# Kernel tuning notes

Hardware: AMD Instinct MI355X
Metric: run time of the kernel (lower is better)

## Reference

```python
import jax, jax.numpy as jnp
import numpy as np

B, S, H, I, E, K = 1, 2048, 1024, 2048, 8, 2


def setup_inputs() -> dict:
    key = jax.random.key(0)
    k0, k1, k2, k3, k4 = jax.random.split(key, 5)
    x = jax.random.normal(k0, (B, S, H), dtype=jnp.float32)
    Wg = jax.random.normal(k1, (H, E), dtype=jnp.float32) * 0.02   # gate (no bias)
    W1 = jax.random.normal(k2, (E, H, I), dtype=jnp.float32) * 0.02  # expert up
    W3 = jax.random.normal(k3, (E, H, I), dtype=jnp.float32) * 0.02  # expert gate
    W2 = jax.random.normal(k4, (E, I, H), dtype=jnp.float32) * 0.02  # expert down
    return {"x": x, "Wg": Wg, "W1": W1, "W2": W2, "W3": W3}


def reference(x, Wg, W1, W2, W3):
    b, s, h = x.shape
    e = Wg.shape[1]
    xf = x.reshape(-1, h)                      # (T, H)
    T = xf.shape[0]

    # Router: top-2 logits, softmax over the 2 selected logits (fp32), cast back.
    logits = xf @ Wg                           # (T, E)
    top_vals, top_idx = jax.lax.top_k(logits, K)
    rw = jax.nn.softmax(top_vals.astype(jnp.float32), axis=-1).astype(x.dtype)  # (T, K)

    # Dense per-expert combine weight: w[t, e] = routing weight if expert e selected, else 0.
    w = jnp.zeros((T, e), dtype=x.dtype).at[jnp.arange(T)[:, None], top_idx].add(rw)

    # Expert MLPs computed for all experts, zero-weighted tokens contribute nothing
    # (mathematically identical to the gather/MLP/scatter-add in the torch loop).
    up = jnp.einsum('th,ehi->tei', xf, W1)     # (T, E, I)
    gate = jnp.einsum('th,ehi->tei', xf, W3)   # (T, E, I)
    act = jax.nn.silu(up) * gate               # (T, E, I)
    out = jnp.einsum('tei,eih,te->th', act, W2, w)  # (T, H)
    return out.reshape(b, s, h)
```

## Files before the change

kernel.cpp:

```cpp
#include <hip/hip_runtime.h>
#include <math.h>

#define NUM_TOK 2048
#define HDIM 1024
#define IDIM 2048
#define NEXP 8
#define MAX_ROWS 6144

typedef __attribute__((ext_vector_type(8))) short bf16x8;
typedef __attribute__((ext_vector_type(4))) float f32x4;

#define OFF_IDX   0u
#define OFF_RW    16384u
#define OFF_SEG   32832u
#define OFF_ROWS  33024u
#define OFF_POS   57600u
#define OFF_XB    131072u
#define OFF_SO    8388608u
#define OFF_ACT   41943040u

__device__ __forceinline__ unsigned short f2bf(float f) {
  __bf16 b = (__bf16)f;
  return __builtin_bit_cast(unsigned short, b);
}

__device__ __forceinline__ unsigned pk2(float lo, float hi) {
  __bf16 a = (__bf16)lo, b = (__bf16)hi;
  return (unsigned)__builtin_bit_cast(unsigned short, a) |
         ((unsigned)__builtin_bit_cast(unsigned short, b) << 16);
}

__device__ __forceinline__ void gld16(const void* g, void* l) {
  __builtin_amdgcn_global_load_lds(
      (const __attribute__((address_space(1))) void*)g,
      (__attribute__((address_space(3))) void*)l, 16, 0, 0);
}

__global__ void k_router(const float* __restrict__ x, const float* __restrict__ wg,
                         unsigned short* __restrict__ xb,
                         int* __restrict__ idx, float* __restrict__ rw) {
  const int wave = threadIdx.x >> 6, lane = threadIdx.x & 63;
  const int t = blockIdx.x * 4 + wave;
  const float2* __restrict__ xr = (const float2*)(x + (size_t)t * HDIM);
  unsigned* __restrict__ xbr = (unsigned*)(xb + (size_t)t * HDIM);
  float acc[8];
#pragma unroll
  for (int q = 0; q < 8; ++q) acc[q] = 0.f;
#pragma unroll
  for (int j = 0; j < 8; ++j) {
    const int h2 = lane + (j << 6);
    const float2 v = xr[h2];
    const float* wrow = wg + (size_t)h2 * 16;
    const float4 a0 = *(const float4*)(wrow);
    const float4 a1 = *(const float4*)(wrow + 4);
    const float4 b0 = *(const float4*)(wrow + 8);
    const float4 b1 = *(const float4*)(wrow + 12);
    acc[0] = fmaf(v.x, a0.x, fmaf(v.y, b0.x, acc[0]));
    acc[1] = fmaf(v.x, a0.y, fmaf(v.y, b0.y, acc[1]));
    acc[2] = fmaf(v.x, a0.z, fmaf(v.y, b0.z, acc[2]));
    acc[3] = fmaf(v.x, a0.w, fmaf(v.y, b0.w, acc[3]));
    acc[4] = fmaf(v.x, a1.x, fmaf(v.y, b1.x, acc[4]));
    acc[5] = fmaf(v.x, a1.y, fmaf(v.y, b1.y, acc[5]));
    acc[6] = fmaf(v.x, a1.z, fmaf(v.y, b1.z, acc[6]));
    acc[7] = fmaf(v.x, a1.w, fmaf(v.y, b1.w, acc[7]));
    xbr[h2] = pk2(v.x, v.y);
  }
#pragma unroll
  for (int q = 0; q < 8; ++q) {
#pragma unroll
    for (int off = 32; off >= 1; off >>= 1)
      acc[q] += __shfl_xor(acc[q], off, 64);
  }
  if (lane == 0) {
    int i0 = 0; float v0 = acc[0];
#pragma unroll
    for (int q = 1; q < 8; ++q)
      if (acc[q] > v0) { v0 = acc[q]; i0 = q; }
    int i1 = -1; float v1 = -3.4e38f;
#pragma unroll
    for (int q = 0; q < 8; ++q)
      if (q != i0 && acc[q] > v1) { v1 = acc[q]; i1 = q; }
    const float e1 = expf(v1 - v0);
    const float inv = 1.f / (1.f + e1);
    idx[2 * t] = i0; idx[2 * t + 1] = i1;
    rw[2 * t] = inv; rw[2 * t + 1] = e1 * inv;
  }
}

__global__ void k_segscatter(const int* __restrict__ idx, int* __restrict__ seg,
                             int* __restrict__ rowsv, int* __restrict__ pos) {
  __shared__ int hist[NEXP], cur[NEXP], sseg[NEXP];
  const int tid = threadIdx.x;
  if (tid < NEXP) { hist[tid] = 0; cur[tid] = 0; }
  __syncthreads();
  for (int s = tid; s < 2 * NUM_TOK; s += 256) atomicAdd(&hist[idx[s]], 1);
  for (int r = tid; r < MAX_ROWS; r += 256) rowsv[r] = -1;
  __syncthreads();
  if (tid == 0) {
    int s = 0;
    for (int q = 0; q < NEXP; ++q) {
      seg[q] = s; sseg[q] = s;
      s += ((hist[q] + 255) / 256) * 256;
    }
    seg[NEXP] = s;
  }
  __syncthreads();
  for (int s = tid; s < 2 * NUM_TOK; s += 256) {
    const int e = idx[s];
    const int p = atomicAdd(&cur[e], 1);
    const int rr = sseg[e] + p;
    rowsv[rr] = s;
    pos[s] = rr;
  }
}

__launch_bounds__(512, 4)
__global__ void k_gemm1(const unsigned short* __restrict__ xb,
                        const float* __restrict__ W1f,
                        const float* __restrict__ W3f,
                        const int* __restrict__ seg, const int* __restrict__ rowsv,
                        unsigned short* __restrict__ act) {
  __shared__ __align__(16) unsigned short As[2][256 * 32];
  __shared__ __align__(16) unsigned short Bs[2][128 * 32];
  const int tid = threadIdx.x;
  const int w = tid >> 6, l = tid & 63;
  const int m0 = blockIdx.y * 256;
  const int total = seg[NEXP];
  if (m0 >= total) return;
  int e = 0;
#pragma unroll
  for (int q = 1; q < NEXP; ++q) if (m0 >= seg[q]) e = q;
  const int n0 = blockIdx.x * 64;

  const int swzA = ((tid & 3) ^ ((tid >> 4) & 3) ^ ((tid >> 3) & 3)) * 8;
  size_t aOff[2];
#pragma unroll
  for (int q = 0; q < 2; ++q) {
    const int r = rowsv[m0 + q * 128 + (tid >> 2)];
    const int tk = (r < 0) ? 0 : (r >> 1);
    aOff[q] = (size_t)tk * HDIM + swzA;
  }
  auto stageA = [&](int buf, int k0) {
#pragma unroll
    for (int q = 0; q < 2; ++q)
      gld16(xb + aOff[q] + k0, &As[buf][(q * 128 + (tid >> 2)) * 32 + (tid & 3) * 8]);
  };

  const int s  = tid >> 8;
  const int kk = (tid >> 4) & 15;
  const int ng = tid & 15;
  const float* __restrict__ Wf = s ? W3f : W1f;
  const size_t bBase = (size_t)e * HDIM * IDIM + (size_t)(2 * kk) * IDIM + n0 + ng * 4;

  struct Bregs { float4 v0, v1; };
  auto loadB = [&](Bregs& p, int k0) {
    const size_t b = bBase + (size_t)k0 * IDIM;
    p.v0 = *(const float4*)(Wf + b);
    p.v1 = *(const float4*)(Wf + b + IDIM);
  };
  auto writeB = [&](int buf, const Bregs& p) {
    unsigned* Bd = (unsigned*)&Bs[buf][0];
    const float a0[4] = {p.v0.x, p.v0.y, p.v0.z, p.v0.w};
    const float a1[4] = {p.v1.x, p.v1.y, p.v1.z, p.v1.w};
#pragma unroll
    for (int i = 0; i < 4; ++i) {
      const int r = s * 64 + ng * 4 + i;
      const int f = ((r >> 2) & 3) ^ ((r >> 1) & 3);
      const int d = (((kk >> 2) ^ f) << 2) + (kk & 3);
      Bd[r * 16 + d] = pk2(a0[i], a1[i]);
    }
  };

  f32x4 acc[2][8];
#pragma unroll
  for (int m = 0; m < 2; ++m)
#pragma unroll
    for (int nf = 0; nf < 8; ++nf) acc[m][nf] = (f32x4)0.f;

  const int rslot = ((l >> 4) ^ ((l >> 2) & 3) ^ ((l >> 1) & 3)) * 8;
  const int arow = (w * 32 + (l & 15)) * 32 + rslot;
  auto mfmaStep = [&](int buf) {
    const bf16x8 a0 = *(const bf16x8*)&As[buf][arow];
    const bf16x8 a1 = *(const bf16x8*)&As[buf][arow + 16 * 32];
#pragma unroll
    for (int nf = 0; nf < 8; ++nf) {
      const bf16x8 b = *(const bf16x8*)&Bs[buf][(nf * 16 + (l & 15)) * 32 + rslot];
      acc[0][nf] = __builtin_amdgcn_mfma_f32_16x16x32_bf16(a0, b, acc[0][nf], 0, 0, 0);
      acc[1][nf] = __builtin_amdgcn_mfma_f32_16x16x32_bf16(a1, b, acc[1][nf], 0, 0, 0);
    }
  };

  Bregs pA, pB;
  loadB(pA, 0);
  stageA(0, 0);
  loadB(pB, 32);
  writeB(0, pA);
  __syncthreads();

  const int NT = HDIM / 32;
  for (int t = 0; t < NT; t += 2) {
    if (t + 2 < NT) loadB(pA, (t + 2) * 32);
    stageA(1, (t + 1) * 32);
    __builtin_amdgcn_sched_barrier(0);
    mfmaStep(0);
    writeB(1, pB);
    __syncthreads();
    if (t + 3 < NT) loadB(pB, (t + 3) * 32);
    if (t + 2 < NT) stageA(0, (t + 2) * 32);
    __builtin_amdgcn_sched_barrier(0);
    mfmaStep(1);
    if (t + 2 < NT) writeB(0, pA);
    __syncthreads();
  }

  const int rbase = m0 + w * 32 + (l >> 4) * 4;
  const int cbase = n0 + (l & 15);
#pragma unroll
  for (int m = 0; m < 2; ++m)
#pragma unroll
    for (int p = 0; p < 4; ++p) {
      const f32x4 up = acc[m][p];
      const f32x4 gt = acc[m][p + 4];
#pragma unroll
      for (int r = 0; r < 4; ++r) {
        const float u = up[r];
        const float sv = (u / (1.f + expf(-u))) * gt[r];
        act[(size_t)(rbase + m * 16 + r) * IDIM + cbase + p * 16] = f2bf(sv);
      }
    }
}

__launch_bounds__(256, 2)
__global__ void k_gemm2(const unsigned short* __restrict__ act,
                        const float* __restrict__ W2f,
                        const int* __restrict__ seg,
                        float* __restrict__ so) {
  __shared__ __align__(16) unsigned short As[2][128 * 32];
  __shared__ __align__(16) unsigned short Bs[2][128 * 32];
  const int tid = threadIdx.x;
  const int w = tid >> 6, l = tid & 63;
  const int m0 = blockIdx.y * 128;
  const int total = seg[NEXP];
  if (m0 >= total) return;
  int e = 0;
#pragma unroll
  for (int q = 1; q < NEXP; ++q) if (m0 >= seg[q]) e = q;
  const int n0 = blockIdx.x * 128;

  const int swzA = ((tid & 3) ^ ((tid >> 4) & 3) ^ ((tid >> 3) & 3)) * 8;
  size_t aOff[2];
#pragma unroll
  for (int q = 0; q < 2; ++q)
    aOff[q] = (size_t)(m0 + q * 64 + (tid >> 2)) * IDIM + swzA;

  const int kk = tid >> 4;
  const int ng = tid & 15;
  const size_t bBase = (size_t)e * IDIM * HDIM + (size_t)(2 * kk) * HDIM + n0 + ng * 4;

  struct Bregs { float4 a0, a1, b0, b1; };
  auto loadB = [&](Bregs& p, int k0) {
    const size_t b = bBase + (size_t)k0 * HDIM;
    p.a0 = *(const float4*)(W2f + b);
    p.a1 = *(const float4*)(W2f + b + HDIM);
    p.b0 = *(const float4*)(W2f + b + 64);
    p.b1 = *(const float4*)(W2f + b + HDIM + 64);
  };
  auto writeB = [&](int buf, const Bregs& p) {
    unsigned* Bd = (unsigned*)&Bs[buf][0];
    const float q00[4] = {p.a0.x, p.a0.y, p.a0.z, p.a0.w};
    const float q01[4] = {p.a1.x, p.a1.y, p.a1.z, p.a1.w};
    const float q10[4] = {p.b0.x, p.b0.y, p.b0.z, p.b0.w};
    const float q11[4] = {p.b1.x, p.b1.y, p.b1.z, p.b1.w};
#pragma unroll
    for (int i = 0; i < 4; ++i) {
      const int rm = ng * 4 + i;
      const int f = ((rm >> 2) & 3) ^ ((rm >> 1) & 3);
      const int d = (((kk >> 2) ^ f) << 2) + (kk & 3);
      Bd[rm * 16 + d]        = pk2(q00[i], q01[i]);
      Bd[(rm + 64) * 16 + d] = pk2(q10[i], q11[i]);
    }
  };
  auto stageA = [&](int buf, int k0) {
#pragma unroll
    for (int q = 0; q < 2; ++q)
      gld16(act + aOff[q] + k0, &As[buf][(q * 64 + (tid >> 2)) * 32]);
  };

  f32x4 acc[2][8];
#pragma unroll
  for (int mf = 0; mf < 2; ++mf)
#pragma unroll
    for (int nf = 0; nf < 8; ++nf) acc[mf][nf] = (f32x4)0.f;

  const int rslot = ((l >> 4) ^ ((l >> 2) & 3) ^ ((l >> 1) & 3)) * 8;
  const int arow = (w * 32 + (l & 15)) * 32 + rslot;
  auto mfmaStep = [&](int buf) {
    const bf16x8 a0 = *(const bf16x8*)&As[buf][arow];
    const bf16x8 a1 = *(const bf16x8*)&As[buf][arow + 16 * 32];
#pragma unroll
    for (int nf = 0; nf < 8; ++nf) {
      const bf16x8 b = *(const bf16x8*)&Bs[buf][(nf * 16 + (l & 15)) * 32 + rslot];
      acc[0][nf] = __builtin_amdgcn_mfma_f32_16x16x32_bf16(a0, b, acc[0][nf], 0, 0, 0);
      acc[1][nf] = __builtin_amdgcn_mfma_f32_16x16x32_bf16(a1, b, acc[1][nf], 0, 0, 0);
    }
  };

  Bregs pA, pB;
  loadB(pA, 0);
  stageA(0, 0);
  loadB(pB, 32);
  writeB(0, pA);
  __syncthreads();

  const int NT = IDIM / 32;
  for (int t = 0; t < NT; t += 2) {
    if (t + 2 < NT) loadB(pA, (t + 2) * 32);
    stageA(1, (t + 1) * 32);
    __builtin_amdgcn_sched_barrier(0);
    mfmaStep(0);
    writeB(1, pB);
    __syncthreads();
    if (t + 3 < NT) loadB(pB, (t + 3) * 32);
    if (t + 2 < NT) stageA(0, (t + 2) * 32);
    __builtin_amdgcn_sched_barrier(0);
    mfmaStep(1);
    if (t + 2 < NT) writeB(0, pA);
    __syncthreads();
  }
  const int rbase = m0 + w * 32 + (l >> 4) * 4;
  const int cbase = n0 + (l & 15);
#pragma unroll
  for (int mf = 0; mf < 2; ++mf)
#pragma unroll
    for (int nf = 0; nf < 8; ++nf)
#pragma unroll
      for (int r = 0; r < 4; ++r)
        so[(size_t)(rbase + mf * 16 + r) * HDIM + cbase + nf * 16] = acc[mf][nf][r];
}

__global__ void k_combine(const float* __restrict__ so, const int* __restrict__ pos,
                          const float* __restrict__ rw, float* __restrict__ out) {
  const int t = blockIdx.x, i = threadIdx.x;
  const int p0 = pos[2 * t], p1 = pos[2 * t + 1];
  const float w0 = rw[2 * t], w1 = rw[2 * t + 1];
  const float4 a = ((const float4*)(so + (size_t)p0 * HDIM))[i];
  const float4 b = ((const float4*)(so + (size_t)p1 * HDIM))[i];
  float4 o;
  o.x = w0 * a.x + w1 * b.x;
  o.y = w0 * a.y + w1 * b.y;
  o.z = w0 * a.z + w1 * b.z;
  o.w = w0 * a.w + w1 * b.w;
  ((float4*)(out + (size_t)t * HDIM))[i] = o;
}

extern "C" void kernel_launch(void* const* d_in, const int* in_sizes, int n_in,
                              void* d_out, int out_size, void* d_ws, size_t ws_size,
                              hipStream_t stream) {
  const float* x  = (const float*)d_in[0];
  const float* Wg = (const float*)d_in[1];
  const float* W1 = (const float*)d_in[2];
  const float* W2 = (const float*)d_in[3];
  const float* W3 = (const float*)d_in[4];
  float* out = (float*)d_out;
  char* ws = (char*)d_ws;
  int*   idx  = (int*)(ws + OFF_IDX);
  float* rw   = (float*)(ws + OFF_RW);
  int*   seg  = (int*)(ws + OFF_SEG);
  int*   rowsv= (int*)(ws + OFF_ROWS);
  int*   pos  = (int*)(ws + OFF_POS);
  unsigned short* xb  = (unsigned short*)(ws + OFF_XB);
  unsigned short* act = (unsigned short*)(ws + OFF_ACT);
  float* so = (float*)(ws + OFF_SO);

  k_router<<<NUM_TOK / 4, 256, 0, stream>>>(x, Wg, xb, idx, rw);
  k_segscatter<<<1, 256, 0, stream>>>(idx, seg, rowsv, pos);
  k_gemm1<<<dim3(IDIM / 64, MAX_ROWS / 256), 512, 0, stream>>>(xb, W1, W3, seg, rowsv, act);
  k_gemm2<<<dim3(HDIM / 128, MAX_ROWS / 128), 256, 0, stream>>>(act, W2, seg, so);
  k_combine<<<NUM_TOK, 256, 0, stream>>>(so, pos, rw, out);
}
```

Before: 161.6 us.

## Fuse weighted combine into down-projection epilogue via atomic adds

Removes the separate combine kernel and the fp32 per-slot intermediate buffer. The second GEMM now scatters routing-weighted results straight into the output with atomicAdd, and a new zero-fill kernel clears the output first. Both GEMM main loops are also reordered so the A staging and B register-to-LDS writes are issued before the MFMA step, and the last half-iteration skips the barrier. The trade-off is many fp32 atomics to global memory, an extra launch, and float summation order that is no longer deterministic.

```diff
diff --git a/kernel.cpp b/kernel.cpp
--- a/kernel.cpp
+++ b/kernel.cpp
@@ -14,9 +14,7 @@
 #define OFF_RW    16384u
 #define OFF_SEG   32832u
 #define OFF_ROWS  33024u
-#define OFF_POS   57600u
 #define OFF_XB    131072u
-#define OFF_SO    8388608u
 #define OFF_ACT   41943040u
 
 __device__ __forceinline__ unsigned short f2bf(float f) {
@@ -34,6 +32,11 @@
   __builtin_amdgcn_global_load_lds(
       (const __attribute__((address_space(1))) void*)g,
       (__attribute__((address_space(3))) void*)l, 16, 0, 0);
+}
+
+__global__ void k_zero(float* __restrict__ out) {
+  const int i = blockIdx.x * blockDim.x + threadIdx.x;
+  ((float4*)out)[i] = make_float4(0.f, 0.f, 0.f, 0.f);
 }
 
 __global__ void k_router(const float* __restrict__ x, const float* __restrict__ wg,
@@ -88,7 +91,7 @@
 }
 
 __global__ void k_segscatter(const int* __restrict__ idx, int* __restrict__ seg,
-                             int* __restrict__ rowsv, int* __restrict__ pos) {
+                             int* __restrict__ rowsv) {
   __shared__ int hist[NEXP], cur[NEXP], sseg[NEXP];
   const int tid = threadIdx.x;
   if (tid < NEXP) { hist[tid] = 0; cur[tid] = 0; }
@@ -108,9 +111,7 @@
   for (int s = tid; s < 2 * NUM_TOK; s += 256) {
     const int e = idx[s];
     const int p = atomicAdd(&cur[e], 1);
-    const int rr = sseg[e] + p;
-    rowsv[rr] = s;
-    pos[s] = rr;
+    rowsv[sseg[e] + p] = s;
   }
 }
 
@@ -199,18 +200,23 @@
 
   const int NT = HDIM / 32;
   for (int t = 0; t < NT; t += 2) {
+    stageA(1, (t + 1) * 32);
     if (t + 2 < NT) loadB(pA, (t + 2) * 32);
-    stageA(1, (t + 1) * 32);
+    writeB(1, pB);
     __builtin_amdgcn_sched_barrier(0);
     mfmaStep(0);
-    writeB(1, pB);
     __syncthreads();
-    if (t + 3 < NT) loadB(pB, (t + 3) * 32);
-    if (t + 2 < NT) stageA(0, (t + 2) * 32);
-    __builtin_amdgcn_sched_barrier(0);
-    mfmaStep(1);
-    if (t + 2 < NT) writeB(0, pA);
-    __syncthreads();
+    if (t + 2 < NT) {
+      stageA(0, (t + 2) * 32);
+      if (t + 3 < NT) loadB(pB, (t + 3) * 32);
+      writeB(0, pA);
+      __builtin_amdgcn_sched_barrier(0);
+      mfmaStep(1);
+      __syncthreads();
+    } else {
+      __builtin_amdgcn_sched_barrier(0);
+      mfmaStep(1);
+    }
   }
 
   const int rbase = m0 + w * 32 + (l >> 4) * 4;
@@ -233,8 +239,9 @@
 __launch_bounds__(256, 2)
 __global__ void k_gemm2(const unsigned short* __restrict__ act,
                         const float* __restrict__ W2f,
-                        const int* __restrict__ seg,
-                        float* __restrict__ so) {
+                        const int* __restrict__ seg, const int* __restrict__ rowsv,
+                        const float* __restrict__ rw,
+                        float* __restrict__ out) {
   __shared__ __align__(16) unsigned short As[2][128 * 32];
   __shared__ __align__(16) unsigned short Bs[2][128 * 32];
   const int tid = threadIdx.x;
@@ -314,43 +321,41 @@
 
   const int NT = IDIM / 32;
   for (int t = 0; t < NT; t += 2) {
+    stageA(1, (t + 1) * 32);
     if (t + 2 < NT) loadB(pA, (t + 2) * 32);
-    stageA(1, (t + 1) * 32);
+    writeB(1, pB);
     __builtin_amdgcn_sched_barrier(0);
     mfmaStep(0);
-    writeB(1, pB);
     __syncthreads();
-    if (t + 3 < NT) loadB(pB, (t + 3) * 32);
-    if (t + 2 < NT) stageA(0, (t + 2) * 32);
-    __builtin_amdgcn_sched_barrier(0);
-    mfmaStep(1);
-    if (t + 2 < NT) writeB(0, pA);
-    __syncthreads();
-  }
+    if (t + 2 < NT) {
+      stageA(0, (t + 2) * 32);
+      if (t + 3 < NT) loadB(pB, (t + 3) * 32);
+      writeB(0, pA);
+      __builtin_amdgcn_sched_barrier(0);
+      mfmaStep(1);
+      __syncthreads();
+    } else {
+      __builtin_amdgcn_sched_barrier(0);
+      mfmaStep(1);
+    }
+  }
+
   const int rbase = m0 + w * 32 + (l >> 4) * 4;
   const int cbase = n0 + (l & 15);
 #pragma unroll
   for (int mf = 0; mf < 2; ++mf)
 #pragma unroll
-    for (int nf = 0; nf < 8; ++nf)
-#pragma unroll
-      for (int r = 0; r < 4; ++r)
-        so[(size_t)(rbase + mf * 16 + r) * HDIM + cbase + nf * 16] = acc[mf][nf][r];
-}
-
-__global__ void k_combine(const float* __restrict__ so, const int* __restrict__ pos,
-                          const float* __restrict__ rw, float* __restrict__ out) {
-  const int t = blockIdx.x, i = threadIdx.x;
-  const int p0 = pos[2 * t], p1 = pos[2 * t + 1];
-  const float w0 = rw[2 * t], w1 = rw[2 * t + 1];
-  const float4 a = ((const float4*)(so + (size_t)p0 * HDIM))[i];
-  const float4 b = ((const float4*)(so + (size_t)p1 * HDIM))[i];
-  float4 o;
-  o.x = w0 * a.x + w1 * b.x;
-  o.y = w0 * a.y + w1 * b.y;
-  o.z = w0 * a.z + w1 * b.z;
-  o.w = w0 * a.w + w1 * b.w;
-  ((float4*)(out + (size_t)t * HDIM))[i] = o;
+    for (int r = 0; r < 4; ++r) {
+      const int row = rbase + mf * 16 + r;
+      const int slot = rowsv[row];
+      if (slot >= 0) {
+        const float wgt = rw[slot];
+        float* op = out + (size_t)(slot >> 1) * HDIM + cbase;
+#pragma unroll
+        for (int nf = 0; nf < 8; ++nf)
+          atomicAdd(op + nf * 16, acc[mf][nf][r] * wgt);
+      }
+    }
 }
 
 extern "C" void kernel_launch(void* const* d_in, const int* in_sizes, int n_in,
@@ -367,14 +372,12 @@
   float* rw   = (float*)(ws + OFF_RW);
   int*   seg  = (int*)(ws + OFF_SEG);
   int*   rowsv= (int*)(ws + OFF_ROWS);
-  int*   pos  = (int*)(ws + OFF_POS);
   unsigned short* xb  = (unsigned short*)(ws + OFF_XB);
   unsigned short* act = (unsigned short*)(ws + OFF_ACT);
-  float* so = (float*)(ws + OFF_SO);
-
+
+  k_zero<<<2048, 256, 0, stream>>>(out);
   k_router<<<NUM_TOK / 4, 256, 0, stream>>>(x, Wg, xb, idx, rw);
-  k_segscatter<<<1, 256, 0, stream>>>(idx, seg, rowsv, pos);
+  k_segscatter<<<1, 256, 0, stream>>>(idx, seg, rowsv);
   k_gemm1<<<dim3(IDIM / 64, MAX_ROWS / 256), 512, 0, stream>>>(xb, W1, W3, seg, rowsv, act);
-  k_gemm2<<<dim3(HDIM / 128, MAX_ROWS / 128), 256, 0, stream>>>(act, W2, seg, so);
-  k_combine<<<NUM_TOK, 256, 0, stream>>>(so, pos, rw, out);
-}
+  k_gemm2<<<dim3(HDIM / 128, MAX_ROWS / 128), 256, 0, stream>>>(act, W2, seg, rowsv, rw, out);
+}
```

Measured after the change: 497.6 us. 208% more time.
